# Kernel tuning notes

Measured on AMD Instinct MI355X. Metric: run time of the kernel, lower is better.

## Reference

```python
import jax, jax.numpy as jnp
import numpy as np

NEG_SLOPE = 0.2   # PyG GATConv default negative_slope
LN_EPS = 1e-5
SOFTMAX_EPS = 1e-16  # PyG softmax denominator eps


def setup_inputs() -> dict:
    key = jax.random.key(0)
    ks = jax.random.split(key, 6)
    N, IN, OUT, H, E = 100000, 128, 64, 2, 1600000
    X = jax.random.normal(ks[0], (N, IN), dtype=jnp.float32)
    edge_index = jax.random.randint(ks[1], (2, E), 0, N, dtype=jnp.int64)
    W = jax.random.normal(ks[2], (H * OUT, IN), dtype=jnp.float32) * 0.05
    att_src = jax.random.normal(ks[3], (H, OUT), dtype=jnp.float32) * 0.05
    att_dst = jax.random.normal(ks[4], (H, OUT), dtype=jnp.float32) * 0.05
    bias = jnp.zeros((OUT,), dtype=jnp.float32)
    ln_gamma = jnp.ones((OUT,), dtype=jnp.float32)
    ln_beta = jnp.zeros((OUT,), dtype=jnp.float32)
    return {"X": X, "edge_index": edge_index, "W": W, "att_src": att_src,
            "att_dst": att_dst, "bias": bias, "ln_gamma": ln_gamma, "ln_beta": ln_beta}


def reference(X, edge_index, W, att_src, att_dst, bias, ln_gamma, ln_beta):
    N = X.shape[0]
    H, F = att_src.shape
    # PyG GATConv default: add self-loops
    loops = jnp.arange(N, dtype=edge_index.dtype)
    src = jnp.concatenate([edge_index[0], loops])  # [Et]
    dst = jnp.concatenate([edge_index[1], loops])  # [Et]
    # linear projection: x' = X @ W^T  -> [N, H, F]
    x = (X @ W.T).reshape(N, H, F)
    # per-node attention logits  [N, H]
    a_src = jnp.einsum('nhf,hf->nh', x, att_src)
    a_dst = jnp.einsum('nhf,hf->nh', x, att_dst)
    # per-edge logits, leaky relu  [Et, H]
    e = jax.nn.leaky_relu(a_src[src] + a_dst[dst], NEG_SLOPE)
    # segment softmax over incoming edges of each dst node
    m = jax.ops.segment_max(e, dst, num_segments=N)          # [N, H]
    ex = jnp.exp(e - m[dst])
    denom = jax.ops.segment_sum(ex, dst, num_segments=N)     # [N, H]
    alpha = ex / (denom[dst] + SOFTMAX_EPS)                  # [Et, H]
    # weighted scatter-add of source features
    msg = x[src] * alpha[:, :, None]                         # [Et, H, F]
    out = jax.ops.segment_sum(msg, dst, num_segments=N)      # [N, H, F]
    # concat=False -> mean over heads, then bias
    out = out.mean(axis=1) + bias                            # [N, F]
    # LayerNorm over features
    mu = out.mean(axis=-1, keepdims=True)
    var = ((out - mu) ** 2).mean(axis=-1, keepdims=True)
    h = (out - mu) * jax.lax.rsqrt(var + LN_EPS) * ln_gamma + ln_beta
    return h
```

## Files before the change

### kernel.cpp

```cpp
#include <hip/hip_runtime.h>
#include <hip/hip_bf16.h>

#define NEG_SLOPE 0.2f
#define LN_EPS 1e-5f
#define SM_EPS 1e-16f

typedef __attribute__((ext_vector_type(8))) short bf16x8;
typedef __attribute__((ext_vector_type(4))) float f32x4;

__device__ inline unsigned short f2bf(float f) {
    unsigned u = __float_as_uint(f);
    return (unsigned short)((u + 0x7FFFu + ((u >> 16) & 1u)) >> 16);
}
__device__ inline float bf_lo(unsigned int v) { return __uint_as_float(v << 16); }
__device__ inline float bf_hi(unsigned int v) { return __uint_as_float(v & 0xffff0000u); }

#define NBIN 512
#define BCAP 4864
#define SCHUNK 4096
#define CURPAD 16

__global__ __launch_bounds__(256) void k_gs(const float* __restrict__ X,
                                            const float* __restrict__ W,
                                            const float* __restrict__ att_src,
                                            const float* __restrict__ att_dst,
                                            unsigned int* __restrict__ xp,
                                            float4* __restrict__ PS,
                                            float4* __restrict__ PD,
                                            const int* __restrict__ ei,
                                            int* __restrict__ binCursor,
                                            unsigned int* __restrict__ tmp,
                                            int N, int E, int SB) {
    __shared__ __align__(16) char smem[52224];
    const int t = threadIdx.x;

    if ((int)blockIdx.x < SB) {
        int* off = (int*)smem;
        const int base = blockIdx.x * SCHUNK;

        int bn[16];
        unsigned int pe[16];
#pragma unroll
        for (int k = 0; k < 16; ++k) {
            int i = base + k * 256 + t;
            if (i < E) {
                int s = ei[i];
                int d = ei[E + i];
                bn[k] = d >> 8;
                pe[k] = ((unsigned)(d & 255) << 24) | (unsigned)s;
            } else {
                bn[k] = -1;
            }
        }

        for (int i = t; i < NBIN; i += 256) off[i] = 0;
        __syncthreads();
#pragma unroll
        for (int k = 0; k < 16; ++k)
            if (bn[k] >= 0) atomicAdd(&off[bn[k]], 1);
        __syncthreads();
        for (int i = t; i < NBIN; i += 256) {
            int h = off[i];
            off[i] = h ? (atomicAdd(&binCursor[i * CURPAD], h) + i * BCAP) : 0;
        }
        __syncthreads();
#pragma unroll
        for (int k = 0; k < 16; ++k) {
            if (bn[k] >= 0) {
                int p = atomicAdd(&off[bn[k]], 1);
                tmp[p] = pe[k];
            }
        }
        return;
    }

    unsigned short* Ws = (unsigned short*)smem;
    unsigned short* Xs = (unsigned short*)(smem + 34816);
    const int b0 = ((int)blockIdx.x - SB) * 64;
    const int lane = t & 63;
    const int w = t >> 6;
    const int c15 = lane & 15;
    const int quad = lane >> 4;

#pragma unroll
    for (int i = 0; i < 16; ++i) {
        int f = i * 256 + t;
        int nr = f >> 5;
        int q = f & 31;
        float4 v = reinterpret_cast<const float4*>(W)[nr * 32 + q];
        ushort4 b;
        b.x = f2bf(v.x); b.y = f2bf(v.y); b.z = f2bf(v.z); b.w = f2bf(v.w);
        *reinterpret_cast<ushort4*>(&Ws[nr * 136 + q * 4]) = b;
    }
#pragma unroll
    for (int i = 0; i < 8; ++i) {
        int f = i * 256 + t;
        int m = f >> 5;
        int q = f & 31;
        int gr = b0 + m;
        if (gr >= N) gr = N - 1;
        float4 v = reinterpret_cast<const float4*>(X)[(size_t)gr * 32 + q];
        ushort4 b;
        b.x = f2bf(v.x); b.y = f2bf(v.y); b.z = f2bf(v.z); b.w = f2bf(v.w);
        *reinterpret_cast<ushort4*>(&Xs[m * 136 + q * 4]) = b;
    }
    __syncthreads();

    f32x4 acc[8];
#pragma unroll
    for (int ct = 0; ct < 8; ++ct) acc[ct] = (f32x4){0.f, 0.f, 0.f, 0.f};

#pragma unroll
    for (int kc = 0; kc < 4; ++kc) {
        bf16x8 af = *reinterpret_cast<const bf16x8*>(
            &Xs[(w * 16 + c15) * 136 + kc * 32 + quad * 8]);
#pragma unroll
        for (int ct = 0; ct < 8; ++ct) {
            bf16x8 bfr = *reinterpret_cast<const bf16x8*>(
                &Ws[(ct * 16 + c15) * 136 + kc * 32 + quad * 8]);
            acc[ct] = __builtin_amdgcn_mfma_f32_16x16x32_bf16(af, bfr, acc[ct], 0, 0, 0);
        }
    }

    float attS[8], attD[8];
#pragma unroll
    for (int ct = 0; ct < 8; ++ct) {
        attS[ct] = att_src[ct * 16 + c15];
        attD[ct] = att_dst[ct * 16 + c15];
    }

#pragma unroll
    for (int r = 0; r < 4; ++r) {
        int row = b0 + w * 16 + quad * 4 + r;
        float s0 = 0.f, s1 = 0.f, d0 = 0.f, d1 = 0.f;
#pragma unroll
        for (int ct = 0; ct < 4; ++ct) {
            s0 += acc[ct][r] * attS[ct];
            d0 += acc[ct][r] * attD[ct];
            s1 += acc[ct + 4][r] * attS[ct + 4];
            d1 += acc[ct + 4][r] * attD[ct + 4];
        }
#pragma unroll
        for (int o = 1; o < 16; o <<= 1) {
            s0 += __shfl_xor(s0, o);
            s1 += __shfl_xor(s1, o);
            d0 += __shfl_xor(d0, o);
            d1 += __shfl_xor(d1, o);
        }
        if (row < N) {
#pragma unroll
            for (int ct = 0; ct < 4; ++ct) {
                unsigned int p = (unsigned int)f2bf(acc[ct][r]) |
                                 ((unsigned int)f2bf(acc[ct + 4][r]) << 16);
                xp[(size_t)row * 64 + ct * 16 + c15] = p;
            }
            if (c15 == 0) {
                PS[row] = make_float4(__expf(s0), __expf(NEG_SLOPE * s0),
                                      __expf(s1), __expf(NEG_SLOPE * s1));
                PD[row] = make_float4(__expf(d0), __expf(NEG_SLOPE * d0),
                                      __expf(d1), __expf(NEG_SLOPE * d1));
            }
        }
    }
}

__global__ __launch_bounds__(512) void k_bucket(const unsigned int* __restrict__ tmp,
                                                const int* __restrict__ binCursor,
                                                unsigned int* __restrict__ csr,
                                                unsigned int* __restrict__ rowPtr,
                                                int N) {
    __shared__ int cnt[256];
    __shared__ int cur[256];
    __shared__ int lds[4];
    const int t = threadIdx.x;
    const int b = blockIdx.x;
    const int start = b * BCAP;
    int m = binCursor[b * CURPAD];
    if (m > BCAP) m = BCAP;

    if (t < 256) cnt[t] = 0;
    __syncthreads();

    for (int k = t; k < m; k += 512) {
        atomicAdd(&cnt[tmp[start + k] >> 24], 1);
    }
    __syncthreads();

    const int lane = t & 63, w = t >> 6;
    int v = 0, incl = 0;
    if (t < 256) {
        v = cnt[t];
        incl = v;
#pragma unroll
        for (int o = 1; o < 64; o <<= 1) {
            int u = __shfl_up(incl, o);
            if (lane >= o) incl += u;
        }
        if (lane == 63) lds[w] = incl;
    }
    __syncthreads();
    if (t == 0) {
        int run = 0;
        for (int i = 0; i < 4; ++i) { int tv = lds[i]; lds[i] = run; run += tv; }
    }
    __syncthreads();
    if (t < 256) {
        int excl = lds[w] + incl - v;
        cur[t] = excl;
        int d = b * 256 + t;
        if (d < N) rowPtr[d] = (unsigned)(start + excl) | ((unsigned)v << 22);
    }
    __syncthreads();

    for (int k = t; k < m; k += 512) {
        unsigned int e = tmp[start + k];
        int p = atomicAdd(&cur[e >> 24], 1);
        csr[start + p] = e & 0x00FFFFFFu;
    }
}

__global__ __launch_bounds__(256) void k_agg(const unsigned int* __restrict__ xp,
                                             const float4* __restrict__ PS,
                                             const float4* __restrict__ PD,
                                             const unsigned int* __restrict__ rowPtr,
                                             const unsigned int* __restrict__ csr,
                                             const float* __restrict__ bias,
                                             const float* __restrict__ gamma,
                                             const float* __restrict__ beta,
                                             float* __restrict__ out, int N) {
    const int w = threadIdx.x >> 6, lane = threadIdx.x & 63;
    const int n = blockIdx.x * 4 + w;
    if (n >= N) return;

    float4 pd = PD[n];
    float4 pss = PS[n];

    float sm0 = pss.x * pd.x, smp0 = pss.y * pd.y;
    float sm1 = pss.z * pd.z, smp1 = pss.w * pd.w;
    float us0 = (sm0 >= 1.f) ? sm0 : smp0;
    float us1 = (sm1 >= 1.f) ? sm1 : smp1;

    unsigned int vself = xp[((unsigned)n << 6) | lane];
    float S0 = us0 * bf_lo(vself);
    float S1 = us1 * bf_hi(vself);
    float D0 = us0, D1 = us1;

    unsigned int pr = rowPtr[n];
    const int jb = (int)(pr & 0x3FFFFFu);
    const int deg = (int)(pr >> 22);
    const int je = jb + deg;
    const int nb = (deg + 7) >> 3;

    const int eq = lane & 7;

    float Dacc0 = 0.f, Dacc1 = 0.f;
    int j = jb;
    unsigned int cc[8];
    unsigned int myc = 0;
    float4 psv = make_float4(0.f, 0.f, 0.f, 0.f);

    if (nb > 0) {
        int ju = __builtin_amdgcn_readfirstlane(jb);
        int last = __builtin_amdgcn_readfirstlane(je - 1);
#pragma unroll
        for (int q = 0; q < 8; ++q) {
            int idx = ju + q; if (idx > last) idx = last;
            cc[q] = csr[idx];
        }
        int mi = ju + eq; if (mi > last) mi = last;
        myc = csr[mi];
        psv = PS[myc];
    }

    for (int bI = 0; bI < nb; ++bI) {
        const int limit = je - j;
        unsigned int v[8];
#pragma unroll
        for (int q = 0; q < 8; ++q)
            v[q] = (xp + ((size_t)cc[q] << 6))[lane];
        unsigned int cn[8], mn;
        {
            int jn = (bI + 1 < nb) ? (j + 8) : jb;
            int ju = __builtin_amdgcn_readfirstlane(jn);
            int last = __builtin_amdgcn_readfirstlane(je - 1);
#pragma unroll
            for (int q = 0; q < 8; ++q) {
                int idx = ju + q; if (idx > last) idx = last;
                cn[q] = csr[idx];
            }
            int mi = ju + eq; if (mi > last) mi = last;
            mn = csr[mi];
        }
        float4 psn = PS[mn];

        float m0 = psv.x * pd.x, mp0 = psv.y * pd.y;
        float m1 = psv.z * pd.z, mp1 = psv.w * pd.w;
        float u0 = (m0 >= 1.f) ? m0 : mp0;
        float u1 = (m1 >= 1.f) ? m1 : mp1;
        unsigned int u01;
        asm("v_cvt_pk_bf16_f32 %0, %1, %2" : "=v"(u01) : "v"(u0), "v"(u1));
        u01 = (eq < limit) ? u01 : 0u;
        Dacc0 += bf_lo(u01);
        Dacc1 += bf_hi(u01);

#pragma unroll
        for (int q = 0; q < 8; ++q) {
            unsigned int ub = (unsigned)__builtin_amdgcn_readlane((int)u01, q);
            float w0 = __uint_as_float(ub << 16);
            float w1 = __uint_as_float(ub & 0xffff0000u);
            S0 = fmaf(w0, bf_lo(v[q]), S0);
            S1 = fmaf(w1, bf_hi(v[q]), S1);
        }
#pragma unroll
        for (int q = 0; q < 8; ++q) cc[q] = cn[q];
        myc = mn;
        psv = psn;
        j += 8;
    }

    Dacc0 += __shfl_xor(Dacc0, 1);
    Dacc0 += __shfl_xor(Dacc0, 2);
    Dacc0 += __shfl_xor(Dacc0, 4);
    Dacc1 += __shfl_xor(Dacc1, 1);
    Dacc1 += __shfl_xor(Dacc1, 2);
    Dacc1 += __shfl_xor(Dacc1, 4);
    D0 += Dacc0;
    D1 += Dacc1;

    float o = (0.5f / (D0 + SM_EPS)) * S0 + (0.5f / (D1 + SM_EPS)) * S1 + bias[lane];

    float mu = o;
#pragma unroll
    for (int d = 32; d > 0; d >>= 1) mu += __shfl_xor(mu, d);
    mu *= (1.0f / 64.0f);
    float dv = o - mu;
    float var = dv * dv;
#pragma unroll
    for (int d = 32; d > 0; d >>= 1) var += __shfl_xor(var, d);
    var *= (1.0f / 64.0f);
    out[(size_t)n * 64 + lane] = dv * rsqrtf(var + LN_EPS) * gamma[lane] + beta[lane];
}

extern "C" void kernel_launch(void* const* d_in, const int* in_sizes, int n_in,
                              void* d_out, int out_size, void* d_ws, size_t ws_size,
                              hipStream_t stream) {
    const float* X        = (const float*)d_in[0];
    const int*   ei       = (const int*)d_in[1];
    const float* W        = (const float*)d_in[2];
    const float* att_src  = (const float*)d_in[3];
    const float* att_dst  = (const float*)d_in[4];
    const float* bias     = (const float*)d_in[5];
    const float* ln_gamma = (const float*)d_in[6];
    const float* ln_beta  = (const float*)d_in[7];
    float* out = (float*)d_out;

    const int N = in_sizes[0] / 128;
    const int E = in_sizes[1] / 2;
    const int NBUCK = (N + 255) / 256;
    const int SB = (E + SCHUNK - 1) / SCHUNK;
    const int GB = (N + 63) / 64;

    char* ws = (char*)d_ws;
    size_t off = 0;
    auto alloc = [&](size_t bytes) {
        size_t o = off;
        off += (bytes + 255) & ~(size_t)255;
        return o;
    };
    unsigned int* xp     = (unsigned int*)(ws + alloc((size_t)N * 64 * 4));
    float4* PS           = (float4*)(ws + alloc((size_t)N * 16));
    float4* PD           = (float4*)(ws + alloc((size_t)N * 16));
    unsigned int* rowPtr = (unsigned int*)(ws + alloc((size_t)N * 4));
    unsigned int* csr    = (unsigned int*)(ws + alloc((size_t)NBIN * BCAP * 4));
    unsigned int* tmp    = (unsigned int*)(ws + alloc((size_t)NBIN * BCAP * 4));
    int* binCursor       = (int*)(ws + alloc(NBIN * CURPAD * 4));

    hipMemsetAsync(binCursor, 0, (size_t)NBIN * CURPAD * 4, stream);
    k_gs<<<SB + GB, 256, 0, stream>>>(X, W, att_src, att_dst, xp, PS, PD,
                                      ei, binCursor, tmp, N, E, SB);
    k_bucket<<<NBUCK, 512, 0, stream>>>(tmp, binCursor, csr, rowPtr, N);
    k_agg<<<(N + 3) / 4, 256, 0, stream>>>(xp, PS, PD, rowPtr, csr,
                                           bias, ln_gamma, ln_beta, out, N);
}
```

Baseline: 219.2 us.

## Precompute edge attention weights and softmax denominators in the bucket kernel

```diff
diff --git a/kernel.cpp b/kernel.cpp
--- a/kernel.cpp
+++ b/kernel.cpp
@@ -164,25 +164,56 @@
     }
 }
 
-__global__ __launch_bounds__(512) void k_bucket(const unsigned int* __restrict__ tmp,
-                                                const int* __restrict__ binCursor,
-                                                unsigned int* __restrict__ csr,
-                                                unsigned int* __restrict__ rowPtr,
-                                                int N) {
+__global__ __launch_bounds__(1024) void k_bucket(const unsigned int* __restrict__ tmp,
+                                                 const int* __restrict__ binCursor,
+                                                 const float4* __restrict__ PS,
+                                                 const float4* __restrict__ PD,
+                                                 uint2* __restrict__ csr,
+                                                 unsigned int* __restrict__ rowPtr,
+                                                 float4* __restrict__ metaN,
+                                                 int N) {
     __shared__ int cnt[256];
     __shared__ int cur[256];
     __shared__ int lds[4];
+    __shared__ float den0[256], den1[256];
+    __shared__ float4 pdc[256];
     const int t = threadIdx.x;
     const int b = blockIdx.x;
     const int start = b * BCAP;
+    const int d0 = b * 256;
     int m = binCursor[b * CURPAD];
     if (m > BCAP) m = BCAP;
 
-    if (t < 256) cnt[t] = 0;
-    __syncthreads();
-
-    for (int k = t; k < m; k += 512) {
-        atomicAdd(&cnt[tmp[start + k] >> 24], 1);
+    if (t < 256) {
+        cnt[t] = 0; den0[t] = 0.f; den1[t] = 0.f;
+        int d = d0 + t;
+        pdc[t] = (d < N) ? PD[d] : make_float4(0.f, 0.f, 0.f, 0.f);
+    }
+    __syncthreads();
+
+    unsigned int ee[5], uu[5];
+#pragma unroll
+    for (int it = 0; it < 5; ++it) {
+        int k = t + it * 1024;
+        ee[it] = 0xFFFFFFFFu;
+        if (k < m) {
+            unsigned int e = tmp[start + k];
+            ee[it] = e;
+            int li = e >> 24;
+            int s = (int)(e & 0x00FFFFFFu);
+            float4 ps = PS[s];
+            float4 pd = pdc[li];
+            float m0 = ps.x * pd.x, mp0 = ps.y * pd.y;
+            float m1 = ps.z * pd.z, mp1 = ps.w * pd.w;
+            float u0 = (m0 >= 1.f) ? m0 : mp0;
+            float u1 = (m1 >= 1.f) ? m1 : mp1;
+            unsigned int u01;
+            asm("v_cvt_pk_bf16_f32 %0, %1, %2" : "=v"(u01) : "v"(u0), "v"(u1));
+            uu[it] = u01;
+            atomicAdd(&cnt[li], 1);
+            atomicAdd(&den0[li], bf_lo(u01));
+            atomicAdd(&den1[li], bf_hi(u01));
+        }
     }
     __syncthreads();
 
@@ -207,23 +238,36 @@
     if (t < 256) {
         int excl = lds[w] + incl - v;
         cur[t] = excl;
-        int d = b * 256 + t;
-        if (d < N) rowPtr[d] = (unsigned)(start + excl) | ((unsigned)v << 22);
-    }
-    __syncthreads();
-
-    for (int k = t; k < m; k += 512) {
-        unsigned int e = tmp[start + k];
-        int p = atomicAdd(&cur[e >> 24], 1);
-        csr[start + p] = e & 0x00FFFFFFu;
+        int d = d0 + t;
+        if (d < N) {
+            rowPtr[d] = (unsigned)(start + excl) | ((unsigned)v << 22);
+            float4 ps = PS[d];
+            float4 pd = pdc[t];
+            float sm0 = ps.x * pd.x, smp0 = ps.y * pd.y;
+            float sm1 = ps.z * pd.z, smp1 = ps.w * pd.w;
+            float us0 = (sm0 >= 1.f) ? sm0 : smp0;
+            float us1 = (sm1 >= 1.f) ? sm1 : smp1;
+            float D0 = den0[t] + us0, D1 = den1[t] + us1;
+            metaN[d] = make_float4(us0, us1,
+                                   0.5f / (D0 + SM_EPS), 0.5f / (D1 + SM_EPS));
+        }
+    }
+    __syncthreads();
+
+#pragma unroll
+    for (int it = 0; it < 5; ++it) {
+        if (ee[it] != 0xFFFFFFFFu) {
+            int li = ee[it] >> 24;
+            int p = atomicAdd(&cur[li], 1);
+            csr[start + p] = make_uint2(ee[it] & 0x00FFFFFFu, uu[it]);
+        }
     }
 }
 
 __global__ __launch_bounds__(256) void k_agg(const unsigned int* __restrict__ xp,
-                                             const float4* __restrict__ PS,
-                                             const float4* __restrict__ PD,
+                                             const float4* __restrict__ metaN,
                                              const unsigned int* __restrict__ rowPtr,
-                                             const unsigned int* __restrict__ csr,
+                                             const uint2* __restrict__ csr,
                                              const float* __restrict__ bias,
                                              const float* __restrict__ gamma,
                                              const float* __restrict__ beta,
@@ -232,102 +276,65 @@
     const int n = blockIdx.x * 4 + w;
     if (n >= N) return;
 
-    float4 pd = PD[n];
-    float4 pss = PS[n];
-
-    float sm0 = pss.x * pd.x, smp0 = pss.y * pd.y;
-    float sm1 = pss.z * pd.z, smp1 = pss.w * pd.w;
-    float us0 = (sm0 >= 1.f) ? sm0 : smp0;
-    float us1 = (sm1 >= 1.f) ? sm1 : smp1;
-
+    float4 meta = metaN[n];
     unsigned int vself = xp[((unsigned)n << 6) | lane];
-    float S0 = us0 * bf_lo(vself);
-    float S1 = us1 * bf_hi(vself);
-    float D0 = us0, D1 = us1;
+    float S0 = meta.x * bf_lo(vself);
+    float S1 = meta.y * bf_hi(vself);
 
     unsigned int pr = rowPtr[n];
     const int jb = (int)(pr & 0x3FFFFFu);
-    const int deg = (int)(pr >> 22);
-    const int je = jb + deg;
-    const int nb = (deg + 7) >> 3;
-
-    const int eq = lane & 7;
-
-    float Dacc0 = 0.f, Dacc1 = 0.f;
+    const int je = jb + (int)(pr >> 22);
     int j = jb;
-    unsigned int cc[8];
-    unsigned int myc = 0;
-    float4 psv = make_float4(0.f, 0.f, 0.f, 0.f);
-
-    if (nb > 0) {
-        int ju = __builtin_amdgcn_readfirstlane(jb);
-        int last = __builtin_amdgcn_readfirstlane(je - 1);
+    const int nfull = (je - jb) >> 3;
+
+    uint2 cc[8];
+    if (nfull > 0) {
+        int ju = __builtin_amdgcn_readfirstlane(j);
+#pragma unroll
+        for (int q = 0; q < 8; ++q) cc[q] = csr[ju + q];
+    }
+    for (int bI = 0; bI < nfull; ++bI) {
+        unsigned int v[8];
+#pragma unroll
+        for (int q = 0; q < 8; ++q) v[q] = xp[(cc[q].x << 6) | lane];
+        uint2 cn[8];
+        {
+            int jn = (bI + 1 < nfull) ? (j + 8) : jb;
+            int ju = __builtin_amdgcn_readfirstlane(jn);
+#pragma unroll
+            for (int q = 0; q < 8; ++q) cn[q] = csr[ju + q];
+        }
 #pragma unroll
         for (int q = 0; q < 8; ++q) {
-            int idx = ju + q; if (idx > last) idx = last;
-            cc[q] = csr[idx];
-        }
-        int mi = ju + eq; if (mi > last) mi = last;
-        myc = csr[mi];
-        psv = PS[myc];
-    }
-
-    for (int bI = 0; bI < nb; ++bI) {
-        const int limit = je - j;
-        unsigned int v[8];
-#pragma unroll
-        for (int q = 0; q < 8; ++q)
-            v[q] = (xp + ((size_t)cc[q] << 6))[lane];
-        unsigned int cn[8], mn;
-        {
-            int jn = (bI + 1 < nb) ? (j + 8) : jb;
-            int ju = __builtin_amdgcn_readfirstlane(jn);
-            int last = __builtin_amdgcn_readfirstlane(je - 1);
-#pragma unroll
-            for (int q = 0; q < 8; ++q) {
-                int idx = ju + q; if (idx > last) idx = last;
-                cn[q] = csr[idx];
-            }
-            int mi = ju + eq; if (mi > last) mi = last;
-            mn = csr[mi];
-        }
-        float4 psn = PS[mn];
-
-        float m0 = psv.x * pd.x, mp0 = psv.y * pd.y;
-        float m1 = psv.z * pd.z, mp1 = psv.w * pd.w;
-        float u0 = (m0 >= 1.f) ? m0 : mp0;
-        float u1 = (m1 >= 1.f) ? m1 : mp1;
-        unsigned int u01;
-        asm("v_cvt_pk_bf16_f32 %0, %1, %2" : "=v"(u01) : "v"(u0), "v"(u1));
-        u01 = (eq < limit) ? u01 : 0u;
-        Dacc0 += bf_lo(u01);
-        Dacc1 += bf_hi(u01);
-
-#pragma unroll
-        for (int q = 0; q < 8; ++q) {
-            unsigned int ub = (unsigned)__builtin_amdgcn_readlane((int)u01, q);
-            float w0 = __uint_as_float(ub << 16);
-            float w1 = __uint_as_float(ub & 0xffff0000u);
-            S0 = fmaf(w0, bf_lo(v[q]), S0);
-            S1 = fmaf(w1, bf_hi(v[q]), S1);
+            S0 = fmaf(bf_lo(cc[q].y), bf_lo(v[q]), S0);
+            S1 = fmaf(bf_hi(cc[q].y), bf_hi(v[q]), S1);
         }
 #pragma unroll
         for (int q = 0; q < 8; ++q) cc[q] = cn[q];
-        myc = mn;
-        psv = psn;
         j += 8;
     }
-
-    Dacc0 += __shfl_xor(Dacc0, 1);
-    Dacc0 += __shfl_xor(Dacc0, 2);
-    Dacc0 += __shfl_xor(Dacc0, 4);
-    Dacc1 += __shfl_xor(Dacc1, 1);
-    Dacc1 += __shfl_xor(Dacc1, 2);
-    Dacc1 += __shfl_xor(Dacc1, 4);
-    D0 += Dacc0;
-    D1 += Dacc1;
-
-    float o = (0.5f / (D0 + SM_EPS)) * S0 + (0.5f / (D1 + SM_EPS)) * S1 + bias[lane];
+    for (; j + 3 < je; j += 4) {
+        int ju = __builtin_amdgcn_readfirstlane(j);
+        uint2 c[4];
+#pragma unroll
+        for (int q = 0; q < 4; ++q) c[q] = csr[ju + q];
+        unsigned int v[4];
+#pragma unroll
+        for (int q = 0; q < 4; ++q) v[q] = xp[(c[q].x << 6) | lane];
+#pragma unroll
+        for (int q = 0; q < 4; ++q) {
+            S0 = fmaf(bf_lo(c[q].y), bf_lo(v[q]), S0);
+            S1 = fmaf(bf_hi(c[q].y), bf_hi(v[q]), S1);
+        }
+    }
+    for (; j < je; ++j) {
+        uint2 c = csr[__builtin_amdgcn_readfirstlane(j)];
+        unsigned int vv = xp[(c.x << 6) | lane];
+        S0 = fmaf(bf_lo(c.y), bf_lo(vv), S0);
+        S1 = fmaf(bf_hi(c.y), bf_hi(vv), S1);
+    }
+
+    float o = meta.z * S0 + meta.w * S1 + bias[lane];
 
     float mu = o;
 #pragma unroll
@@ -370,15 +377,17 @@
     unsigned int* xp     = (unsigned int*)(ws + alloc((size_t)N * 64 * 4));
     float4* PS           = (float4*)(ws + alloc((size_t)N * 16));
     float4* PD           = (float4*)(ws + alloc((size_t)N * 16));
+    float4* metaN        = (float4*)(ws + alloc((size_t)N * 16));
     unsigned int* rowPtr = (unsigned int*)(ws + alloc((size_t)N * 4));
-    unsigned int* csr    = (unsigned int*)(ws + alloc((size_t)NBIN * BCAP * 4));
+    uint2* csr           = (uint2*)(ws + alloc((size_t)NBIN * BCAP * 8));
     unsigned int* tmp    = (unsigned int*)(ws + alloc((size_t)NBIN * BCAP * 4));
     int* binCursor       = (int*)(ws + alloc(NBIN * CURPAD * 4));
 
     hipMemsetAsync(binCursor, 0, (size_t)NBIN * CURPAD * 4, stream);
     k_gs<<<SB + GB, 256, 0, stream>>>(X, W, att_src, att_dst, xp, PS, PD,
                                       ei, binCursor, tmp, N, E, SB);
-    k_bucket<<<NBUCK, 512, 0, stream>>>(tmp, binCursor, csr, rowPtr, N);
-    k_agg<<<(N + 3) / 4, 256, 0, stream>>>(xp, PS, PD, rowPtr, csr,
+    k_bucket<<<NBUCK, 1024, 0, stream>>>(tmp, binCursor, PS, PD, csr, rowPtr,
+                                         metaN, N);
+    k_agg<<<(N + 3) / 4, 256, 0, stream>>>(xp, metaN, rowPtr, csr,
                                            bias, ln_gamma, ln_beta, out, N);
 }
```

After: 229.1 us. 1.05x slower.
